# Optimization experiments

Measured on AMD Instinct MI355X. Metric: run time of the kernel, lower is better.

Reference implementation:

```python
import jax, jax.numpy as jnp
import numpy as np

B, S, F, H, Dh = 1, 2048, 1024, 16, 64


def rel_shift(x):
    # x: [qlen, klen, B, H] -- Transformer-XL relative shift
    q, k = x.shape[0], x.shape[1]
    x_padded = jnp.pad(x, ((0, 0), (1, 0), (0, 0), (0, 0)))
    x_padded = x_padded.reshape((k + 1, q) + x.shape[2:])
    return x_padded[1:].reshape(x.shape)


def setup_inputs() -> dict:
    key = jax.random.key(0)
    ks = jax.random.split(key, 14)
    sc = 1.0 / np.sqrt(F)
    return {
        "inputs_q": jax.random.normal(ks[0], (B, S, F), jnp.float32),
        "pos_emb": jax.random.normal(ks[1], (S, F), jnp.float32),
        "r_w_bias": jax.random.normal(ks[2], (H, Dh), jnp.float32) * 0.02,
        "r_r_bias": jax.random.normal(ks[3], (H, Dh), jnp.float32) * 0.02,
        "Wq": jax.random.normal(ks[4], (F, H, Dh), jnp.float32) * sc,
        "bq": jnp.zeros((H, Dh), jnp.float32),
        "Wk": jax.random.normal(ks[5], (F, H, Dh), jnp.float32) * sc,
        "bk": jnp.zeros((H, Dh), jnp.float32),
        "Wv": jax.random.normal(ks[6], (F, H, Dh), jnp.float32) * sc,
        "bv": jnp.zeros((H, Dh), jnp.float32),
        "Wr": jax.random.normal(ks[7], (F, H, Dh), jnp.float32) * sc,
        "br": jnp.zeros((H, Dh), jnp.float32),
        "Wo": jax.random.normal(ks[8], (H, Dh, F), jnp.float32) * (1.0 / np.sqrt(H * Dh)),
        "bo": jnp.zeros((F,), jnp.float32),
    }


def reference(inputs_q, pos_emb, r_w_bias, r_r_bias, Wq, bq, Wk, bk, Wv, bv, Wr, br, Wo, bo):
    # QKV projections: [B,S,F] x [F,H,Dh] -> [B,S,H,Dh]
    q = jnp.einsum('bsf,fhd->bshd', inputs_q, Wq) + bq
    k = jnp.einsum('bsf,fhd->bshd', inputs_q, Wk) + bk
    v = jnp.einsum('bsf,fhd->bshd', inputs_q, Wv) + bv
    # relative position key projection: [S,F] -> [S,H,Dh]
    r_key = jnp.einsum('sf,fhd->shd', pos_emb[-k.shape[1]:], Wr) + br
    # content (AC) and position (BD) score terms, layout [i, j, B, H]
    AC = jnp.einsum('bihd,bjhd->ijbh', q + r_w_bias, k)
    BD = jnp.einsum('bihd,jhd->ijbh', q + r_r_bias, r_key)
    BD = rel_shift(BD)
    depth = jnp.asarray(q.shape[-1], jnp.float32)
    attn_score = ((AC + BD) / jnp.sqrt(depth)).transpose((2, 3, 0, 1))  # [B,H,S,S]
    # causal mask -> additive bias (0 where allowed, -1e10 where disallowed)
    seq = q.shape[1]
    causal = jnp.tril(jnp.ones((seq, seq), dtype=bool))[None, None]
    attn_score = attn_score + jnp.where(causal, 0.0, -1e10).astype(attn_score.dtype)
    probs = jax.nn.softmax(attn_score, axis=-1)
    out = jnp.einsum('bhij,bjhd->bihd', probs, v)  # [B,S,H,Dh]
    return jnp.einsum('bihd,hdf->bif', out, Wo) + bo  # [B,S,F]
```

## Files before the change

### kernel.cpp

```cpp
#include <hip/hip_runtime.h>

#define S 2048
#define F 1024
#define H 16
#define DH 64
#define NH (H * DH)

typedef __attribute__((ext_vector_type(8))) short bf16x8;
typedef __attribute__((ext_vector_type(4))) float f32x4;

__device__ __forceinline__ ushort f2bf(float f) {
  unsigned u = __float_as_uint(f);
  u = (u + 0x7FFFu + ((u >> 16) & 1u)) >> 16;
  return (ushort)u;
}
__device__ __forceinline__ float bf2f(ushort u) {
  return __uint_as_float(((unsigned)u) << 16);
}

__device__ __forceinline__ void gload16(const void* g, void* l) {
  __builtin_amdgcn_global_load_lds(
      (const __attribute__((address_space(1))) void*)g,
      (__attribute__((address_space(3))) void*)l, 16, 0, 0);
}

__device__ __forceinline__ bf16x8 ldsT(const ushort* buf, int row, int kbyte) {
  return *(const bf16x8*)((const char*)buf + row * 128 +
                          (kbyte ^ ((row & 7) << 4)));
}

__global__ __launch_bounds__(256) void conv_bf16(const float* __restrict__ src,
                                                 ushort* __restrict__ dst,
                                                 int n) {
  const int i = (blockIdx.x * 256 + threadIdx.x) * 4;
  if (i < n) {
    const float4 v = *(const float4*)(src + i);
    ushort4 u;
    u.x = f2bf(v.x); u.y = f2bf(v.y); u.z = f2bf(v.z); u.w = f2bf(v.w);
    *(ushort4*)(dst + i) = u;
  }
}

__global__ __launch_bounds__(256) void tconv(const float* __restrict__ src,
                                             ushort* __restrict__ dst) {
  __shared__ ushort T[64][72];
  const int r0 = blockIdx.y * 64, c0 = blockIdx.x * 64;
  const int t = threadIdx.x;
#pragma unroll
  for (int q = 0; q < 4; ++q) {
    const int row = q * 16 + (t >> 4);
    const int col = (t & 15) * 4;
    const float4 v = *(const float4*)(src + (size_t)(r0 + row) * 1024 + c0 + col);
    T[row][col + 0] = f2bf(v.x);
    T[row][col + 1] = f2bf(v.y);
    T[row][col + 2] = f2bf(v.z);
    T[row][col + 3] = f2bf(v.w);
  }
  __syncthreads();
#pragma unroll
  for (int q = 0; q < 4; ++q) {
    const int orow = q * 16 + (t >> 4);
    const int ocol = (t & 15) * 4;
    ushort4 u;
    u.x = T[ocol + 0][orow];
    u.y = T[ocol + 1][orow];
    u.z = T[ocol + 2][orow];
    u.w = T[ocol + 3][orow];
    *(ushort4*)(dst + (size_t)(c0 + orow) * 1024 + r0 + ocol) = u;
  }
}

template <int EPI>
__global__ __launch_bounds__(256, 2) void mm_bf16(
    const ushort* __restrict__ A, const ushort* __restrict__ Bt,
    const float* __restrict__ b0, const float* __restrict__ b1,
    const float* __restrict__ b2, const float* __restrict__ b3,
    const float* __restrict__ b4, void* __restrict__ o0, void* __restrict__ o1,
    void* __restrict__ o2, void* __restrict__ o3, int M, int N, int K) {
  __shared__ __align__(16) ushort Asb[2][64 * 64];
  __shared__ __align__(16) ushort Bsb[2][128 * 64];
  const int tid = threadIdx.x;
  const int l = tid & 63, w = tid >> 6;
  const int wm = w >> 1, wn = w & 1;
  const int m0 = blockIdx.y * 64, n0 = blockIdx.x * 128;

  f32x4 acc[2][4];
#pragma unroll
  for (int m = 0; m < 2; ++m)
#pragma unroll
    for (int n = 0; n < 4; ++n) acc[m][n] = (f32x4){0.f, 0.f, 0.f, 0.f};

#define MM_STAGE(c, kt)                                                        \
  {                                                                            \
    const int k0 = (kt) * 64;                                                  \
    _Pragma("unroll") for (int i = 0; i < 2; ++i) {                            \
      const int LB = (i * 256 + tid) * 16, row = LB >> 7, rb_ = LB & 127;      \
      const int tb = rb_ ^ ((row & 7) << 4);                                   \
      gload16((const char*)A + ((size_t)(m0 + row) * K + k0) * 2 + tb,         \
              (char*)Asb[c] + LB);                                             \
    }                                                                          \
    _Pragma("unroll") for (int i = 0; i < 4; ++i) {                            \
      const int LB = (i * 256 + tid) * 16, row = LB >> 7, rb_ = LB & 127;      \
      const int tb = rb_ ^ ((row & 7) << 4);                                   \
      gload16((const char*)Bt + ((size_t)(n0 + row) * K + k0) * 2 + tb,        \
              (char*)Bsb[c] + LB);                                             \
    }                                                                          \
  }

  MM_STAGE(0, 0);
  __syncthreads();
  const int NT = K >> 6;
  int cur = 0;
  for (int kt = 0; kt < NT; ++kt) {
    if (kt + 1 < NT) MM_STAGE(cur ^ 1, kt + 1);
#pragma unroll
    for (int ks = 0; ks < 2; ++ks) {
      bf16x8 af[2], bfr[4];
#pragma unroll
      for (int m = 0; m < 2; ++m)
        af[m] = ldsT(Asb[cur], wm * 32 + m * 16 + (l & 15),
                     ks * 64 + (l >> 4) * 16);
#pragma unroll
      for (int n = 0; n < 4; ++n)
        bfr[n] = ldsT(Bsb[cur], wn * 64 + n * 16 + (l & 15),
                      ks * 64 + (l >> 4) * 16);
      __builtin_amdgcn_s_setprio(1);
#pragma unroll
      for (int m = 0; m < 2; ++m)
#pragma unroll
        for (int n = 0; n < 4; ++n)
          acc[m][n] = __builtin_amdgcn_mfma_f32_16x16x32_bf16(
              af[m], bfr[n], acc[m][n], 0, 0, 0);
      __builtin_amdgcn_s_setprio(0);
    }
    __syncthreads();
    cur ^= 1;
  }

#pragma unroll
  for (int m = 0; m < 2; ++m)
#pragma unroll
    for (int n = 0; n < 4; ++n) {
      const int colg = n0 + wn * 64 + n * 16 + (l & 15);
      const int rowb = m0 + wm * 32 + m * 16 + (l >> 4) * 4;
      if constexpr (EPI == 0) {
        ushort* C = (ushort*)o0;
        const float bs = b0[colg];
#pragma unroll
        for (int r = 0; r < 4; ++r)
          C[(size_t)(rowb + r) * N + colg] = f2bf(acc[m][n][r] + bs);
      } else if constexpr (EPI == 3) {
        float* C = (float*)o0;
        const float bs = b0[colg];
#pragma unroll
        for (int r = 0; r < 4; ++r)
          C[(size_t)(rowb + r) * N + colg] = acc[m][n][r] + bs;
      } else {
        const int band = colg >> 10;
        const int colm = colg & 1023;
        if (band == 0) {
          const float bs = b0[colm], vw = b1[colm], vr = b2[colm];
          ushort* Cw = (ushort*)o0;
          ushort* Cr = (ushort*)o1;
#pragma unroll
          for (int r = 0; r < 4; ++r) {
            const float v = acc[m][n][r] + bs;
            Cw[(size_t)(rowb + r) * NH + colm] = f2bf(v + vw);
            Cr[(size_t)(rowb + r) * NH + colm] = f2bf(v + vr);
          }
        } else if (band == 1) {
          const float bs = b3[colm];
          ushort* C = (ushort*)o2;
#pragma unroll
          for (int r = 0; r < 4; ++r)
            C[(size_t)(rowb + r) * NH + colm] = f2bf(acc[m][n][r] + bs);
        } else {
          const float bs = b4[colm];
          ushort* C = (ushort*)o3;
          ushort4 u;
          u.x = f2bf(acc[m][n][0] + bs);
          u.y = f2bf(acc[m][n][1] + bs);
          u.z = f2bf(acc[m][n][2] + bs);
          u.w = f2bf(acc[m][n][3] + bs);
          *(ushort4*)(C + (size_t)colm * M + rowb) = u;
        }
      }
    }
}

__global__ __launch_bounds__(256, 2) void attn_mfma(
    const ushort* __restrict__ qw, const ushort* __restrict__ qr,
    const ushort* __restrict__ kb, const ushort* __restrict__ vt,
    const ushort* __restrict__ rb, float* __restrict__ accA,
    float* __restrict__ accB, float* __restrict__ mA, float* __restrict__ lA,
    float* __restrict__ mB, float* __restrict__ lB) {
  __shared__ __align__(16) ushort Kb[2][64 * 64];
  __shared__ __align__(16) ushort Vb[2][64 * 64];
  __shared__ __align__(16) ushort Rb[2][64 * 64];
  __shared__ __align__(16) ushort BDb[2][64 * 64];
  __shared__ __align__(16) ushort Pb[4][16 * 64];

  const int bx = blockIdx.x;
  const int it = 31 - (bx >> 5);
  const int half = (bx >> 4) & 1;
  const int h = bx & 15;
  const int i0 = it * 64;
  const int tid = threadIdx.x;
  const int l = tid & 63, w = tid >> 6;
  const int lo = (it + 1) >> 1;
  const int fr_base = w * 16 + (l >> 4) * 4;

  float* __restrict__ accX = half ? accB : accA;
  float* __restrict__ mX = half ? mB : mA;
  float* __restrict__ lX = half ? lB : lA;

  if (half == 1 && lo == 0) {
#pragma unroll
    for (int n = 0; n < 4; ++n)
#pragma unroll
      for (int r = 0; r < 4; ++r)
        accX[(size_t)(i0 + fr_base + r) * NH + h * 64 + n * 16 + (l & 15)] =
            0.f;
    if ((l & 15) == 0)
#pragma unroll
      for (int r = 0; r < 4; ++r) {
        mX[(i0 + fr_base + r) * H + h] = -1e30f;
        lX[(i0 + fr_base + r) * H + h] = 0.f;
      }
    return;
  }

  const int jstart = half ? (lo - 1) : it;
  const int jend = half ? 0 : lo;
  const int tp0 = it - jstart;

#pragma unroll
  for (int i = 0; i < 2; ++i) {
    const int LB = (i * 256 + tid) * 16, row = LB >> 7, rb_ = LB & 127;
    gload16((const char*)qw + ((size_t)(i0 + row) * NH + h * 64) * 2 + rb_,
            (char*)Kb[0] + LB);
    gload16((const char*)qr + ((size_t)(i0 + row) * NH + h * 64) * 2 + rb_,
            (char*)Kb[1] + LB);
  }
  __syncthreads();
  bf16x8 qwf[2], qrf[2];
#pragma unroll
  for (int ks = 0; ks < 2; ++ks) {
    const int row = w * 16 + (l & 15);
    const int kbyte = ks * 64 + (l >> 4) * 16;
    qwf[ks] = *(const bf16x8*)((const char*)Kb[0] + row * 128 + kbyte);
    qrf[ks] = *(const bf16x8*)((const char*)Kb[1] + row * 128 + kbyte);
  }
  __syncthreads();

  f32x4 acc_o[4];
#pragma unroll
  for (int n = 0; n < 4; ++n) acc_o[n] = (f32x4){0.f, 0.f, 0.f, 0.f};
  f32x4 acc_l = (f32x4){0.f, 0.f, 0.f, 0.f};
  float m_r[4] = {-1e30f, -1e30f, -1e30f, -1e30f};

  const short one_bf = (short)0x3F80;
  const bf16x8 ones = {one_bf, one_bf, one_bf, one_bf,
                       one_bf, one_bf, one_bf, one_bf};

#define AT_STAGE(c, jt_)                                                       \
  {                                                                            \
    const int j0 = (jt_) * 64;                                                 \
    const int tp_ = it - (jt_);                                                \
    _Pragma("unroll") for (int i = 0; i < 2; ++i) {                            \
      const int LB = (i * 256 + tid) * 16, row = LB >> 7, rb_ = LB & 127;      \
      const int tb = rb_ ^ ((row & 7) << 4);                                   \
      gload16((const char*)kb + ((size_t)(j0 + row) * NH + h * 64) * 2 + tb,   \
              (char*)Kb[c] + LB);                                              \
      gload16((const char*)vt + ((size_t)(h * 64 + row) * S + j0) * 2 + tb,    \
              (char*)Vb[c] + LB);                                              \
      gload16((const char*)rb +                                                \
                  ((size_t)(S - 1 - 64 * tp_ - row) * NH + h * 64) * 2 + tb,   \
              (char*)Rb[c] + LB);                                              \
    }                                                                          \
  }

  if (half) {
#pragma unroll
    for (int i = 0; i < 2; ++i) {
      const int LB = (i * 256 + tid) * 16, row = LB >> 7, rb_ = LB & 127;
      const int tb = rb_ ^ ((row & 7) << 4);
      gload16((const char*)rb +
                  ((size_t)(S - 1 - 64 * (tp0 - 1) - row) * NH + h * 64) * 2 +
                  tb,
              (char*)Rb[1] + LB);
    }
  }
  AT_STAGE(0, jstart);
  __syncthreads();
  if (half) {
    f32x4 bd[4];
#pragma unroll
    for (int n = 0; n < 4; ++n) bd[n] = (f32x4){0.f, 0.f, 0.f, 0.f};
#pragma unroll
    for (int ks = 0; ks < 2; ++ks) {
      bf16x8 rf[4];
#pragma unroll
      for (int n = 0; n < 4; ++n)
        rf[n] = ldsT(Rb[1], n * 16 + (l & 15), ks * 64 + (l >> 4) * 16);
      __builtin_amdgcn_s_setprio(1);
#pragma unroll
      for (int n = 0; n < 4; ++n)
        bd[n] = __builtin_amdgcn_mfma_f32_16x16x32_bf16(qrf[ks], rf[n], bd[n],
                                                        0, 0, 0);
      __builtin_amdgcn_s_setprio(0);
    }
    ushort* B = BDb[(tp0 - 1) & 1];
#pragma unroll
    for (int n = 0; n < 4; ++n)
#pragma unroll
      for (int r = 0; r < 4; ++r)
        B[(fr_base + r) * 64 + n * 16 + (l & 15)] = f2bf(bd[n][r]);
    __syncthreads();
  }

  int cur = 0;
  for (int jt = jstart; jt >= jend; --jt) {
    const int tp = it - jt;
    if (jt > jend) AT_STAGE(cur ^ 1, jt - 1);

    f32x4 bd[4];
#pragma unroll
    for (int n = 0; n < 4; ++n) bd[n] = (f32x4){0.f, 0.f, 0.f, 0.f};
#pragma unroll
    for (int ks = 0; ks < 2; ++ks) {
      bf16x8 rf[4];
#pragma unroll
      for (int n = 0; n < 4; ++n)
        rf[n] = ldsT(Rb[cur], n * 16 + (l & 15), ks * 64 + (l >> 4) * 16);
      __builtin_amdgcn_s_setprio(1);
#pragma unroll
      for (int n = 0; n < 4; ++n)
        bd[n] = __builtin_amdgcn_mfma_f32_16x16x32_bf16(qrf[ks], rf[n], bd[n],
                                                        0, 0, 0);
      __builtin_amdgcn_s_setprio(0);
    }
    {
      ushort* B = BDb[tp & 1];
#pragma unroll
      for (int n = 0; n < 4; ++n)
#pragma unroll
        for (int r = 0; r < 4; ++r)
          B[(fr_base + r) * 64 + n * 16 + (l & 15)] = f2bf(bd[n][r]);
    }

    f32x4 sa[4];
#pragma unroll
    for (int n = 0; n < 4; ++n) sa[n] = (f32x4){0.f, 0.f, 0.f, 0.f};
#pragma unroll
    for (int ks = 0; ks < 2; ++ks) {
      bf16x8 kf[4];
#pragma unroll
      for (int n = 0; n < 4; ++n)
        kf[n] = ldsT(Kb[cur], n * 16 + (l & 15), ks * 64 + (l >> 4) * 16);
      __builtin_amdgcn_s_setprio(1);
#pragma unroll
      for (int n = 0; n < 4; ++n)
        sa[n] = __builtin_amdgcn_mfma_f32_16x16x32_bf16(qwf[ks], kf[n], sa[n],
                                                        0, 0, 0);
      __builtin_amdgcn_s_setprio(0);
    }

    const ushort* Bnew = BDb[tp & 1];
    const ushort* Bold = BDb[(tp & 1) ^ 1];
    float p[4][4];
    float rmax[4] = {-1e30f, -1e30f, -1e30f, -1e30f};
#pragma unroll
    for (int n = 0; n < 4; ++n)
#pragma unroll
      for (int r = 0; r < 4; ++r) {
        const int fr = fr_base + r;
        const int jj = n * 16 + (l & 15);
        const int u = 64 + fr - jj;
        const float bdv =
            bf2f((u >= 64) ? Bnew[fr * 64 + (u - 64)] : Bold[fr * 64 + u]);
        float s = (sa[n][r] + bdv) * 0.125f;
        if (tp == 0 && jj > fr) s = -1e30f;
        p[n][r] = s;
        rmax[r] = fmaxf(rmax[r], s);
      }
#pragma unroll
    for (int off = 1; off < 16; off <<= 1)
#pragma unroll
      for (int r = 0; r < 4; ++r)
        rmax[r] = fmaxf(rmax[r], __shfl_xor(rmax[r], off, 64));
    float corr[4];
#pragma unroll
    for (int r = 0; r < 4; ++r) {
      const float mn = fmaxf(m_r[r], rmax[r]);
      corr[r] = __expf(m_r[r] - mn);
      m_r[r] = mn;
    }
#pragma unroll
    for (int n = 0; n < 4; ++n)
#pragma unroll
      for (int r = 0; r < 4; ++r) p[n][r] = __expf(p[n][r] - m_r[r]);
#pragma unroll
    for (int r = 0; r < 4; ++r) acc_l[r] *= corr[r];
#pragma unroll
    for (int n = 0; n < 4; ++n)
#pragma unroll
      for (int r = 0; r < 4; ++r) acc_o[n][r] *= corr[r];

    {
      ushort* P = Pb[w];
#pragma unroll
      for (int n = 0; n < 4; ++n)
#pragma unroll
        for (int r = 0; r < 4; ++r) {
          const int row = (l >> 4) * 4 + r;
          const int colb = (n * 16 + (l & 15)) * 2;
          *(ushort*)((char*)P + row * 128 + (colb ^ ((row & 7) << 4))) =
              f2bf(p[n][r]);
        }
    }

#pragma unroll
    for (int ks = 0; ks < 2; ++ks) {
      const int prow = l & 15;
      const bf16x8 pf = *(const bf16x8*)(
          (const char*)Pb[w] + prow * 128 +
          ((ks * 64 + (l >> 4) * 16) ^ ((prow & 7) << 4)));
      bf16x8 vf[4];
#pragma unroll
      for (int n = 0; n < 4; ++n)
        vf[n] = ldsT(Vb[cur], n * 16 + (l & 15), ks * 64 + (l >> 4) * 16);
      __builtin_amdgcn_s_setprio(1);
#pragma unroll
      for (int n = 0; n < 4; ++n)
        acc_o[n] = __builtin_amdgcn_mfma_f32_16x16x32_bf16(pf, vf[n], acc_o[n],
                                                           0, 0, 0);
      acc_l = __builtin_amdgcn_mfma_f32_16x16x32_bf16(pf, ones, acc_l, 0, 0, 0);
      __builtin_amdgcn_s_setprio(0);
    }
    __syncthreads();
    cur ^= 1;
  }

#pragma unroll
  for (int n = 0; n < 4; ++n)
#pragma unroll
    for (int r = 0; r < 4; ++r)
      accX[(size_t)(i0 + fr_base + r) * NH + h * 64 + n * 16 + (l & 15)] =
          acc_o[n][r];
  if ((l & 15) == 0)
#pragma unroll
    for (int r = 0; r < 4; ++r) {
      mX[(i0 + fr_base + r) * H + h] = m_r[r];
      lX[(i0 + fr_base + r) * H + h] = acc_l[r];
    }
}

__global__ __launch_bounds__(256) void combine_halves(
    const float* __restrict__ accA, const float* __restrict__ accB,
    const float* __restrict__ mA, const float* __restrict__ lA,
    const float* __restrict__ mB, const float* __restrict__ lB,
    ushort* __restrict__ ab) {
  const int idx = blockIdx.x * 256 + threadIdx.x;
  const int base = idx * 4;
  const int i = base >> 10;
  const int h = (base & 1023) >> 6;
  const float4 a = *(const float4*)(accA + base);
  const float4 b = *(const float4*)(accB + base);
  const float ma = mA[i * H + h], la = lA[i * H + h];
  const float mb = mB[i * H + h], lb = lB[i * H + h];
  const float M = fmaxf(ma, mb);
  const float ea = __expf(ma - M), eb = __expf(mb - M);
  const float inv = 1.f / (la * ea + lb * eb);
  ushort4 u;
  u.x = f2bf((a.x * ea + b.x * eb) * inv);
  u.y = f2bf((a.y * ea + b.y * eb) * inv);
  u.z = f2bf((a.z * ea + b.z * eb) * inv);
  u.w = f2bf((a.w * ea + b.w * eb) * inv);
  *(ushort4*)(ab + base) = u;
}

extern "C" void kernel_launch(void* const* d_in, const int* in_sizes, int n_in,
                              void* d_out, int out_size, void* d_ws,
                              size_t ws_size, hipStream_t stream) {
  const float* inq = (const float*)d_in[0];
  const float* pos = (const float*)d_in[1];
  const float* rwb = (const float*)d_in[2];
  const float* rrb = (const float*)d_in[3];
  const float* Wq = (const float*)d_in[4];
  const float* bq = (const float*)d_in[5];
  const float* Wk = (const float*)d_in[6];
  const float* bk = (const float*)d_in[7];
  const float* Wv = (const float*)d_in[8];
  const float* bv = (const float*)d_in[9];
  const float* Wr = (const float*)d_in[10];
  const float* br = (const float*)d_in[11];
  const float* Wo = (const float*)d_in[12];
  const float* bo = (const float*)d_in[13];

  char* ws = (char*)d_ws;
  const size_t MB = 1024 * 1024;
  ushort* A_bf = (ushort*)(ws + 0 * MB);
  ushort* P_bf = (ushort*)(ws + 4 * MB);
  ushort* Wqkv = (ushort*)(ws + 8 * MB);
  ushort* Wrt = (ushort*)(ws + 14 * MB);
  ushort* Wot = (ushort*)(ws + 16 * MB);
  ushort* qwp = (ushort*)(ws + 18 * MB);
  ushort* qrp = (ushort*)(ws + 22 * MB);
  ushort* kbp = (ushort*)(ws + 26 * MB);
  ushort* vtp = (ushort*)(ws + 30 * MB);
  ushort* rbp = (ushort*)(ws + 34 * MB);
  float* mlA = (float*)(ws + 4 * MB);
  float* mA = mlA + 0 * 32768;
  float* lA = mlA + 1 * 32768;
  float* mB = mlA + 2 * 32768;
  float* lB = mlA + 3 * 32768;
  float* accA = (float*)(ws + 6 * MB);
  float* accB = (float*)(ws + 38 * MB);
  ushort* abp = A_bf;

  conv_bf16<<<2048, 256, 0, stream>>>(inq, A_bf, S * F);
  conv_bf16<<<2048, 256, 0, stream>>>(pos, P_bf, S * F);
  const dim3 gt(16, 16);
  tconv<<<gt, 256, 0, stream>>>(Wq, Wqkv);
  tconv<<<gt, 256, 0, stream>>>(Wk, Wqkv + 1024 * 1024);
  tconv<<<gt, 256, 0, stream>>>(Wv, Wqkv + 2048 * 1024);
  tconv<<<gt, 256, 0, stream>>>(Wr, Wrt);
  tconv<<<gt, 256, 0, stream>>>(Wo, Wot);

  mm_bf16<4><<<dim3(24, 32), 256, 0, stream>>>(A_bf, Wqkv, bq, rwb, rrb, bk, bv,
                                               qwp, qrp, kbp, vtp, S, 3072, F);
  mm_bf16<0><<<dim3(8, 32), 256, 0, stream>>>(P_bf, Wrt, br, nullptr, nullptr,
                                              nullptr, nullptr, rbp, nullptr,
                                              nullptr, nullptr, S, NH, F);

  attn_mfma<<<1024, 256, 0, stream>>>(qwp, qrp, kbp, vtp, rbp, accA, accB, mA,
                                      lA, mB, lB);
  combine_halves<<<2048, 256, 0, stream>>>(accA, accB, mA, lA, mB, lB, abp);

  mm_bf16<3><<<dim3(8, 32), 256, 0, stream>>>(abp, Wot, bo, nullptr, nullptr,
                                              nullptr, nullptr, d_out, nullptr,
                                              nullptr, nullptr, S, F, NH);
}
```

Baseline: 214.7 us.

## Fuse prep kernels, merge projection GEMMs with 128x128 tiles, exp2 softmax with lazy rescale

Merges the seven conversion and transpose launches into one prep kernel. Merges the QKV and R projections into a single 128x128-tile GEMM launch using a z dimension. The 1/sqrt(d)*log2(e) scale is folded into the q projection so softmax can use raw v_exp_f32, and rescaling of the running output is skipped unless the row max grows by more than 8. BD shared-memory rows are padded to cut bank conflicts. These cut launch overhead and per-element softmax work, at the cost of higher register use with the larger tiles, and the lazy rescale lets unnormalised values grow by up to 2^8.

Measured after the change: 216.5 us. About the same (+0.9%).

```diff
diff --git a/kernel.cpp b/kernel.cpp
--- a/kernel.cpp
+++ b/kernel.cpp
@@ -9,6 +9,8 @@
 typedef __attribute__((ext_vector_type(8))) short bf16x8;
 typedef __attribute__((ext_vector_type(4))) float f32x4;
 
+#define QSCALE 0.1803368801111244f
+
 __device__ __forceinline__ ushort f2bf(float f) {
   unsigned u = __float_as_uint(f);
   u = (u + 0x7FFFu + ((u >> 16) & 1u)) >> 16;
@@ -17,6 +19,11 @@
 __device__ __forceinline__ float bf2f(ushort u) {
   return __uint_as_float(((unsigned)u) << 16);
 }
+__device__ __forceinline__ float ex2(float x) {
+  float r;
+  asm volatile("v_exp_f32 %0, %1\ns_nop 0" : "=v"(r) : "v"(x));
+  return r;
+}
 
 __device__ __forceinline__ void gload16(const void* g, void* l) {
   __builtin_amdgcn_global_load_lds(
@@ -29,23 +36,38 @@
                           (kbyte ^ ((row & 7) << 4)));
 }
 
-__global__ __launch_bounds__(256) void conv_bf16(const float* __restrict__ src,
-                                                 ushort* __restrict__ dst,
-                                                 int n) {
-  const int i = (blockIdx.x * 256 + threadIdx.x) * 4;
-  if (i < n) {
+__global__ __launch_bounds__(256) void prep(
+    const float* __restrict__ inq, const float* __restrict__ pos,
+    const float* __restrict__ Wq, const float* __restrict__ Wk,
+    const float* __restrict__ Wv, const float* __restrict__ Wr,
+    const float* __restrict__ Wo, ushort* __restrict__ A_bf,
+    ushort* __restrict__ P_bf, ushort* __restrict__ Wqkv,
+    ushort* __restrict__ Wrt, ushort* __restrict__ Wot) {
+  __shared__ ushort T[64][72];
+  const int b = blockIdx.x;
+  const int t = threadIdx.x;
+  if (b < 4096) {
+    const float* src = (b < 2048) ? inq : pos;
+    ushort* dst = (b < 2048) ? A_bf : P_bf;
+    const int i = ((b & 2047) * 256 + t) * 4;
     const float4 v = *(const float4*)(src + i);
     ushort4 u;
     u.x = f2bf(v.x); u.y = f2bf(v.y); u.z = f2bf(v.z); u.w = f2bf(v.w);
     *(ushort4*)(dst + i) = u;
-  }
-}
-
-__global__ __launch_bounds__(256) void tconv(const float* __restrict__ src,
-                                             ushort* __restrict__ dst) {
-  __shared__ ushort T[64][72];
-  const int r0 = blockIdx.y * 64, c0 = blockIdx.x * 64;
-  const int t = threadIdx.x;
+    return;
+  }
+  const int bb = b - 4096;
+  const int which = bb >> 8;
+  const int sub = bb & 255;
+  const float* src = which == 0 ? Wq
+                     : which == 1 ? Wk
+                     : which == 2 ? Wv
+                     : which == 3 ? Wr : Wo;
+  ushort* dst = which == 0 ? Wqkv
+                : which == 1 ? Wqkv + 1024 * 1024
+                : which == 2 ? Wqkv + 2048 * 1024
+                : which == 3 ? Wrt : Wot;
+  const int r0 = (sub >> 4) * 64, c0 = (sub & 15) * 64;
 #pragma unroll
   for (int q = 0; q < 4; ++q) {
     const int row = q * 16 + (t >> 4);
@@ -71,54 +93,57 @@
 }
 
 template <int EPI>
-__global__ __launch_bounds__(256, 2) void mm_bf16(
-    const ushort* __restrict__ A, const ushort* __restrict__ Bt,
-    const float* __restrict__ b0, const float* __restrict__ b1,
-    const float* __restrict__ b2, const float* __restrict__ b3,
-    const float* __restrict__ b4, void* __restrict__ o0, void* __restrict__ o1,
-    void* __restrict__ o2, void* __restrict__ o3, int M, int N, int K) {
-  __shared__ __align__(16) ushort Asb[2][64 * 64];
+__global__ __launch_bounds__(256, 2) void mm128(
+    const ushort* __restrict__ A0, const ushort* __restrict__ A1,
+    const ushort* __restrict__ B0, const ushort* __restrict__ B1,
+    const float* __restrict__ c0, const float* __restrict__ c1,
+    const float* __restrict__ c2, const float* __restrict__ c3,
+    const float* __restrict__ c4, const float* __restrict__ c5,
+    ushort* __restrict__ o0, ushort* __restrict__ o1, ushort* __restrict__ o2,
+    ushort* __restrict__ o3, ushort* __restrict__ o4, float* __restrict__ of) {
+  __shared__ __align__(16) ushort Asb[2][128 * 64];
   __shared__ __align__(16) ushort Bsb[2][128 * 64];
   const int tid = threadIdx.x;
   const int l = tid & 63, w = tid >> 6;
   const int wm = w >> 1, wn = w & 1;
-  const int m0 = blockIdx.y * 64, n0 = blockIdx.x * 128;
-
-  f32x4 acc[2][4];
-#pragma unroll
-  for (int m = 0; m < 2; ++m)
+  const int bz = (EPI == 0) ? blockIdx.z : 0;
+  if (EPI == 0 && bz == 1 && blockIdx.x >= 8) return;
+  const ushort* Ause = (EPI == 0 && bz) ? A1 : A0;
+  const ushort* Buse = (EPI == 0 && bz) ? B1 : B0;
+  const int m0 = blockIdx.y * 128, n0 = blockIdx.x * 128;
+  const int K = 1024;
+
+  f32x4 acc[4][4];
+#pragma unroll
+  for (int m = 0; m < 4; ++m)
 #pragma unroll
     for (int n = 0; n < 4; ++n) acc[m][n] = (f32x4){0.f, 0.f, 0.f, 0.f};
 
-#define MM_STAGE(c, kt)                                                        \
+#define M128_STAGE(c, kt)                                                      \
   {                                                                            \
     const int k0 = (kt) * 64;                                                  \
-    _Pragma("unroll") for (int i = 0; i < 2; ++i) {                            \
-      const int LB = (i * 256 + tid) * 16, row = LB >> 7, rb_ = LB & 127;      \
-      const int tb = rb_ ^ ((row & 7) << 4);                                   \
-      gload16((const char*)A + ((size_t)(m0 + row) * K + k0) * 2 + tb,         \
-              (char*)Asb[c] + LB);                                             \
-    }                                                                          \
     _Pragma("unroll") for (int i = 0; i < 4; ++i) {                            \
       const int LB = (i * 256 + tid) * 16, row = LB >> 7, rb_ = LB & 127;      \
       const int tb = rb_ ^ ((row & 7) << 4);                                   \
-      gload16((const char*)Bt + ((size_t)(n0 + row) * K + k0) * 2 + tb,        \
+      gload16((const char*)Ause + ((size_t)(m0 + row) * K + k0) * 2 + tb,      \
+              (char*)Asb[c] + LB);                                             \
+      gload16((const char*)Buse + ((size_t)(n0 + row) * K + k0) * 2 + tb,      \
               (char*)Bsb[c] + LB);                                             \
     }                                                                          \
   }
 
-  MM_STAGE(0, 0);
+  M128_STAGE(0, 0);
   __syncthreads();
-  const int NT = K >> 6;
   int cur = 0;
-  for (int kt = 0; kt < NT; ++kt) {
-    if (kt + 1 < NT) MM_STAGE(cur ^ 1, kt + 1);
+#pragma unroll 1
+  for (int kt = 0; kt < 16; ++kt) {
+    if (kt + 1 < 16) M128_STAGE(cur ^ 1, kt + 1);
 #pragma unroll
     for (int ks = 0; ks < 2; ++ks) {
-      bf16x8 af[2], bfr[4];
-#pragma unroll
-      for (int m = 0; m < 2; ++m)
-        af[m] = ldsT(Asb[cur], wm * 32 + m * 16 + (l & 15),
+      bf16x8 af[4], bfr[4];
+#pragma unroll
+      for (int m = 0; m < 4; ++m)
+        af[m] = ldsT(Asb[cur], wm * 64 + m * 16 + (l & 15),
                      ks * 64 + (l >> 4) * 16);
 #pragma unroll
       for (int n = 0; n < 4; ++n)
@@ -126,7 +151,7 @@
                       ks * 64 + (l >> 4) * 16);
       __builtin_amdgcn_s_setprio(1);
 #pragma unroll
-      for (int m = 0; m < 2; ++m)
+      for (int m = 0; m < 4; ++m)
 #pragma unroll
         for (int n = 0; n < 4; ++n)
           acc[m][n] = __builtin_amdgcn_mfma_f32_16x16x32_bf16(
@@ -138,51 +163,45 @@
   }
 
 #pragma unroll
-  for (int m = 0; m < 2; ++m)
+  for (int m = 0; m < 4; ++m)
 #pragma unroll
     for (int n = 0; n < 4; ++n) {
+      const int rowb = m0 + wm * 64 + m * 16 + (l >> 4) * 4;
       const int colg = n0 + wn * 64 + n * 16 + (l & 15);
-      const int rowb = m0 + wm * 32 + m * 16 + (l >> 4) * 4;
-      if constexpr (EPI == 0) {
-        ushort* C = (ushort*)o0;
-        const float bs = b0[colg];
+      if constexpr (EPI == 1) {
+        const float bs = c0[colg];
 #pragma unroll
         for (int r = 0; r < 4; ++r)
-          C[(size_t)(rowb + r) * N + colg] = f2bf(acc[m][n][r] + bs);
-      } else if constexpr (EPI == 3) {
-        float* C = (float*)o0;
-        const float bs = b0[colg];
+          of[(size_t)(rowb + r) * 1024 + colg] = acc[m][n][r] + bs;
+      } else if (bz == 1) {
+        const float bs = c5[colg];
 #pragma unroll
         for (int r = 0; r < 4; ++r)
-          C[(size_t)(rowb + r) * N + colg] = acc[m][n][r] + bs;
+          o4[(size_t)(rowb + r) * NH + colg] = f2bf(acc[m][n][r] + bs);
       } else {
         const int band = colg >> 10;
         const int colm = colg & 1023;
         if (band == 0) {
-          const float bs = b0[colm], vw = b1[colm], vr = b2[colm];
-          ushort* Cw = (ushort*)o0;
-          ushort* Cr = (ushort*)o1;
+          const float bs = c0[colm], vw = c1[colm], vr = c2[colm];
 #pragma unroll
           for (int r = 0; r < 4; ++r) {
             const float v = acc[m][n][r] + bs;
-            Cw[(size_t)(rowb + r) * NH + colm] = f2bf(v + vw);
-            Cr[(size_t)(rowb + r) * NH + colm] = f2bf(v + vr);
+            o0[(size_t)(rowb + r) * NH + colm] = f2bf((v + vw) * QSCALE);
+            o1[(size_t)(rowb + r) * NH + colm] = f2bf((v + vr) * QSCALE);
           }
         } else if (band == 1) {
-          const float bs = b3[colm];
-          ushort* C = (ushort*)o2;
+          const float bs = c3[colm];
 #pragma unroll
           for (int r = 0; r < 4; ++r)
-            C[(size_t)(rowb + r) * NH + colm] = f2bf(acc[m][n][r] + bs);
+            o2[(size_t)(rowb + r) * NH + colm] = f2bf(acc[m][n][r] + bs);
         } else {
-          const float bs = b4[colm];
-          ushort* C = (ushort*)o3;
+          const float bs = c4[colm];
           ushort4 u;
           u.x = f2bf(acc[m][n][0] + bs);
           u.y = f2bf(acc[m][n][1] + bs);
           u.z = f2bf(acc[m][n][2] + bs);
           u.w = f2bf(acc[m][n][3] + bs);
-          *(ushort4*)(C + (size_t)colm * M + rowb) = u;
+          *(ushort4*)(o3 + (size_t)colm * S + rowb) = u;
         }
       }
     }
@@ -197,7 +216,7 @@
   __shared__ __align__(16) ushort Kb[2][64 * 64];
   __shared__ __align__(16) ushort Vb[2][64 * 64];
   __shared__ __align__(16) ushort Rb[2][64 * 64];
-  __shared__ __align__(16) ushort BDb[2][64 * 64];
+  __shared__ __align__(16) ushort BDb[2][64 * 68];
   __shared__ __align__(16) ushort Pb[4][16 * 64];
 
   const int bx = blockIdx.x;
@@ -315,7 +334,7 @@
     for (int n = 0; n < 4; ++n)
 #pragma unroll
       for (int r = 0; r < 4; ++r)
-        B[(fr_base + r) * 64 + n * 16 + (l & 15)] = f2bf(bd[n][r]);
+        B[(fr_base + r) * 68 + n * 16 + (l & 15)] = f2bf(bd[n][r]);
     __syncthreads();
   }
 
@@ -346,7 +365,7 @@
       for (int n = 0; n < 4; ++n)
 #pragma unroll
         for (int r = 0; r < 4; ++r)
-          B[(fr_base + r) * 64 + n * 16 + (l & 15)] = f2bf(bd[n][r]);
+          B[(fr_base + r) * 68 + n * 16 + (l & 15)] = f2bf(bd[n][r]);
     }
 
     f32x4 sa[4];
@@ -378,8 +397,8 @@
         const int jj = n * 16 + (l & 15);
         const int u = 64 + fr - jj;
         const float bdv =
-            bf2f((u >= 64) ? Bnew[fr * 64 + (u - 64)] : Bold[fr * 64 + u]);
-        float s = (sa[n][r] + bdv) * 0.125f;
+            bf2f((u >= 64) ? Bnew[fr * 68 + (u - 64)] : Bold[fr * 68 + u]);
+        float s = sa[n][r] + bdv;
         if (tp == 0 && jj > fr) s = -1e30f;
         p[n][r] = s;
         rmax[r] = fmaxf(rmax[r], s);
@@ -389,23 +408,28 @@
 #pragma unroll
       for (int r = 0; r < 4; ++r)
         rmax[r] = fmaxf(rmax[r], __shfl_xor(rmax[r], off, 64));
-    float corr[4];
-#pragma unroll
-    for (int r = 0; r < 4; ++r) {
-      const float mn = fmaxf(m_r[r], rmax[r]);
-      corr[r] = __expf(m_r[r] - mn);
-      m_r[r] = mn;
+    int grow = 0;
+#pragma unroll
+    for (int r = 0; r < 4; ++r) grow |= (rmax[r] > m_r[r] + 8.f);
+    if (__any(grow)) {
+      float corr[4];
+#pragma unroll
+      for (int r = 0; r < 4; ++r) {
+        const float mn = fmaxf(m_r[r], rmax[r]);
+        corr[r] = ex2(m_r[r] - mn);
+        m_r[r] = mn;
+      }
+#pragma unroll
+      for (int r = 0; r < 4; ++r) acc_l[r] *= corr[r];
+#pragma unroll
+      for (int n = 0; n < 4; ++n)
+#pragma unroll
+        for (int r = 0; r < 4; ++r) acc_o[n][r] *= corr[r];
     }
 #pragma unroll
     for (int n = 0; n < 4; ++n)
 #pragma unroll
-      for (int r = 0; r < 4; ++r) p[n][r] = __expf(p[n][r] - m_r[r]);
-#pragma unroll
-    for (int r = 0; r < 4; ++r) acc_l[r] *= corr[r];
-#pragma unroll
-    for (int n = 0; n < 4; ++n)
-#pragma unroll
-      for (int r = 0; r < 4; ++r) acc_o[n][r] *= corr[r];
+      for (int r = 0; r < 4; ++r) p[n][r] = ex2(p[n][r] - m_r[r]);
 
     {
       ushort* P = Pb[w];
@@ -470,7 +494,7 @@
   const float ma = mA[i * H + h], la = lA[i * H + h];
   const float mb = mB[i * H + h], lb = lB[i * H + h];
   const float M = fmaxf(ma, mb);
-  const float ea = __expf(ma - M), eb = __expf(mb - M);
+  const float ea = ex2(ma - M), eb = ex2(mb - M);
   const float inv = 1.f / (la * ea + lb * eb);
   ushort4 u;
   u.x = f2bf((a.x * ea + b.x * eb) * inv);
@@ -519,26 +543,18 @@
   float* accB = (float*)(ws + 38 * MB);
   ushort* abp = A_bf;
 
-  conv_bf16<<<2048, 256, 0, stream>>>(inq, A_bf, S * F);
-  conv_bf16<<<2048, 256, 0, stream>>>(pos, P_bf, S * F);
-  const dim3 gt(16, 16);
-  tconv<<<gt, 256, 0, stream>>>(Wq, Wqkv);
-  tconv<<<gt, 256, 0, stream>>>(Wk, Wqkv + 1024 * 1024);
-  tconv<<<gt, 256, 0, stream>>>(Wv, Wqkv + 2048 * 1024);
-  tconv<<<gt, 256, 0, stream>>>(Wr, Wrt);
-  tconv<<<gt, 256, 0, stream>>>(Wo, Wot);
-
-  mm_bf16<4><<<dim3(24, 32), 256, 0, stream>>>(A_bf, Wqkv, bq, rwb, rrb, bk, bv,
-                                               qwp, qrp, kbp, vtp, S, 3072, F);
-  mm_bf16<0><<<dim3(8, 32), 256, 0, stream>>>(P_bf, Wrt, br, nullptr, nullptr,
-                                              nullptr, nullptr, rbp, nullptr,
-                                              nullptr, nullptr, S, NH, F);
+  prep<<<5376, 256, 0, stream>>>(inq, pos, Wq, Wk, Wv, Wr, Wo, A_bf, P_bf,
+                                 Wqkv, Wrt, Wot);
+
+  mm128<0><<<dim3(24, 16, 2), 256, 0, stream>>>(
+      A_bf, P_bf, Wqkv, Wrt, bq, rwb, rrb, bk, bv, br, qwp, qrp, kbp, vtp, rbp,
+      nullptr);
 
   attn_mfma<<<1024, 256, 0, stream>>>(qwp, qrp, kbp, vtp, rbp, accA, accB, mA,
                                       lA, mB, lB);
   combine_halves<<<2048, 256, 0, stream>>>(accA, accB, mA, lA, mB, lB, abp);
 
-  mm_bf16<3><<<dim3(8, 32), 256, 0, stream>>>(abp, Wot, bo, nullptr, nullptr,
-                                              nullptr, nullptr, d_out, nullptr,
-                                              nullptr, nullptr, S, F, NH);
-}
+  mm128<1><<<dim3(8, 16, 1), 256, 0, stream>>>(
+      abp, nullptr, Wot, nullptr, bo, nullptr, nullptr, nullptr, nullptr,
+      nullptr, nullptr, nullptr, nullptr, nullptr, nullptr, (float*)d_out);
+}
```
